# Kernel optimization log

Hardware: AMD Instinct MI355X
Metric: run time of the kernel (lower is better)

## Reference

```python
import jax, jax.numpy as jnp
import numpy as np

N_HEADS = 16
D_K = 64  # d_model / n_heads = 1024 / 16


def setup_inputs() -> dict:
    key = jax.random.key(0)
    ks = jax.random.split(key, 7)
    B, S, D = 4, 2048, 1024
    scale = 1.0 / np.sqrt(D)
    return {
        "Q": jax.random.normal(ks[0], (B, S, D), dtype=jnp.float32),
        "K": jax.random.normal(ks[1], (B, S, D), dtype=jnp.float32),
        "V": jax.random.normal(ks[2], (B, S, D), dtype=jnp.float32),
        # Linear weights stored as [in, out] so y = x @ W (bias=False in original).
        "WQ": jax.random.normal(ks[3], (D, D), dtype=jnp.float32) * scale,
        "WK": jax.random.normal(ks[4], (D, D), dtype=jnp.float32) * scale,
        "WV": jax.random.normal(ks[5], (D, D), dtype=jnp.float32) * scale,
        "Wfc": jax.random.normal(ks[6], (D, D), dtype=jnp.float32) * scale,
    }


def reference(Q, K, V, WQ, WK, WV, Wfc):
    B = Q.shape[0]
    # NOTE: the original uses a raw reshape [B, S, H*dk] -> [B, H, S, dk]
    # (NOT the usual view+transpose); row-major reshape reproduces it exactly.
    q = (Q @ WQ).reshape(B, N_HEADS, -1, D_K)  # [B, H, S, dk]
    k = (K @ WK).reshape(B, N_HEADS, -1, D_K)
    v = (V @ WV).reshape(B, N_HEADS, -1, D_K)
    scores = jnp.einsum("bhqd,bhkd->bhqk", q, k) / jnp.sqrt(jnp.asarray(D_K, q.dtype))
    attn = jax.nn.softmax(scores, axis=-1)
    ctx = jnp.einsum("bhqk,bhkd->bhqd", attn, v)  # [B, H, S, dk]
    ctx = jnp.transpose(ctx, (0, 2, 1, 3)).reshape(B, -1, N_HEADS * D_K)  # [B, S, D]
    return ctx @ Wfc
```

## Files before the change

kernel.cpp:

```cpp
#include <hip/hip_runtime.h>
#include <stdint.h>
#include <math.h>


typedef __attribute__((ext_vector_type(8))) short short8;
typedef __attribute__((ext_vector_type(4))) float f32x4;
typedef __attribute__((ext_vector_type(16))) float f32x16;
typedef __attribute__((ext_vector_type(2))) unsigned int u32x2;
typedef __attribute__((ext_vector_type(4))) unsigned int u32x4;
typedef __attribute__((ext_vector_type(8))) _Float16 half8;

__device__ __forceinline__ unsigned short bf16rne(float f) {
  unsigned int u = __builtin_bit_cast(unsigned int, f);
  unsigned int r = u + 0x7FFFu + ((u >> 16) & 1u);
  return (unsigned short)(r >> 16);
}

__device__ __forceinline__ void gld_lds16(const void* g, void* l) {
  typedef __attribute__((address_space(3))) unsigned int lds_u32;
  typedef const __attribute__((address_space(1))) unsigned int glb_u32;
  __builtin_amdgcn_global_load_lds((glb_u32*)(uintptr_t)g,
                                   (lds_u32*)(unsigned int)(uintptr_t)l,
                                   16, 0, 0);
}

__device__ __forceinline__ unsigned pkrtz(float a, float b) {
  auto h = __builtin_amdgcn_cvt_pkrtz(a, b);
  return __builtin_bit_cast(unsigned, h);
}

__device__ __forceinline__ float fexp2(float x) {
#if __has_builtin(__builtin_amdgcn_exp2f)
  return __builtin_amdgcn_exp2f(x);
#else
  float r;
  asm("v_exp_f32 %0, %1" : "=v"(r) : "v"(x));
  return r;
#endif
}

__global__ void convert_x_kernel(const float* __restrict__ Q,
                                 const float* __restrict__ K,
                                 const float* __restrict__ V,
                                 unsigned short* __restrict__ Xb) {
  const int z = blockIdx.y;
  const float* src = (z == 0) ? Q : (z == 1) ? K : V;
  const size_t i0 = ((size_t)blockIdx.x * 256 + threadIdx.x) * 8;
  const f32x4 a = *(const f32x4*)(src + i0);
  const f32x4 c = *(const f32x4*)(src + i0 + 4);
  u32x4 o;
  o[0] = (unsigned)bf16rne(a[0]) | ((unsigned)bf16rne(a[1]) << 16);
  o[1] = (unsigned)bf16rne(a[2]) | ((unsigned)bf16rne(a[3]) << 16);
  o[2] = (unsigned)bf16rne(c[0]) | ((unsigned)bf16rne(c[1]) << 16);
  o[3] = (unsigned)bf16rne(c[2]) | ((unsigned)bf16rne(c[3]) << 16);
  *(u32x4*)(Xb + (size_t)z * 8388608 + i0) = o;
}

__global__ void convert_w_kernel(const float* __restrict__ W0,
                                 const float* __restrict__ W1,
                                 const float* __restrict__ W2,
                                 const float* __restrict__ W3,
                                 unsigned short* __restrict__ Wt) {
  const int z = blockIdx.z;
  const float* W = (z == 0) ? W0 : (z == 1) ? W1 : (z == 2) ? W2 : W3;
  unsigned short* dst = Wt + (size_t)z * 1048576;
  __shared__ float tile[32][33];
  const int tx = threadIdx.x & 31, ty = threadIdx.x >> 5;
  const int k0 = blockIdx.x * 32, n0 = blockIdx.y * 32;
#pragma unroll
  for (int yy = 0; yy < 32; yy += 8)
    tile[ty + yy][tx] = W[(size_t)(k0 + ty + yy) * 1024 + n0 + tx];
  __syncthreads();
#pragma unroll
  for (int yy = 0; yy < 32; yy += 8)
    dst[(size_t)(n0 + ty + yy) * 1024 + k0 + tx] = bf16rne(tile[tx][ty + yy]);
}

__global__ __launch_bounds__(256, 2) void gemm_bt_kernel(
    const unsigned short* __restrict__ A, const unsigned short* __restrict__ Bt,
    unsigned short* __restrict__ Cbf, float* __restrict__ Cf32, float scaleZ0) {
  constexpr int K = 1024, N = 1024;
  const int z = blockIdx.z;
  const unsigned short* Ab = A + (size_t)z * 8192 * 1024;
  const unsigned short* Bb = Bt + (size_t)z * 1024 * 1024;
  const int tid = threadIdx.x;
  const int lane = tid & 63;
  const int w = tid >> 6;
  const int l15 = lane & 15, quad = lane >> 4;
  const int rowBase = blockIdx.x * 128;
  const int colBase = blockIdx.y * 128;
  const int wrow = (w >> 1) * 64;
  const int wcol = (w & 1) * 64;
  __shared__ __align__(16) unsigned short As[128 * 32];
  __shared__ __align__(16) unsigned short Bs[128 * 32];

  const f32x4 z4 = {0.0f, 0.0f, 0.0f, 0.0f};
  f32x4 acc[4][4];
#pragma unroll
  for (int i = 0; i < 4; i++)
#pragma unroll
    for (int j = 0; j < 4; j++) acc[i][j] = z4;

  const int s0 = tid, s1 = tid + 256;
  const int rA0 = s0 >> 2, cA0 = (s0 & 3) * 8;
  const int rA1 = s1 >> 2, cA1 = (s1 & 3) * 8;

  for (int k0 = 0; k0 < K; k0 += 32) {
    gld_lds16(Ab + (size_t)(rowBase + rA0) * K + k0 + cA0, (void*)(As + s0 * 8));
    gld_lds16(Ab + (size_t)(rowBase + rA1) * K + k0 + cA1, (void*)(As + s1 * 8));
    gld_lds16(Bb + (size_t)(colBase + rA0) * K + k0 + cA0, (void*)(Bs + s0 * 8));
    gld_lds16(Bb + (size_t)(colBase + rA1) * K + k0 + cA1, (void*)(Bs + s1 * 8));
    __syncthreads();
    short8 af[4], bfr[4];
#pragma unroll
    for (int i = 0; i < 4; i++)
      af[i] = *(const short8*)(As + (wrow + i * 16 + l15) * 32 + quad * 8);
#pragma unroll
    for (int j = 0; j < 4; j++)
      bfr[j] = *(const short8*)(Bs + (wcol + j * 16 + l15) * 32 + quad * 8);
#pragma unroll
    for (int i = 0; i < 4; i++)
#pragma unroll
      for (int j = 0; j < 4; j++)
        acc[i][j] =
            __builtin_amdgcn_mfma_f32_16x16x32_bf16(af[i], bfr[j], acc[i][j], 0, 0, 0);
    __syncthreads();
  }

  const float sc = (z == 0) ? scaleZ0 : 1.0f;
#pragma unroll
  for (int i = 0; i < 4; i++) {
#pragma unroll
    for (int j = 0; j < 4; j++) {
#pragma unroll
      for (int r = 0; r < 4; r++) {
        const int row = rowBase + wrow + i * 16 + quad * 4 + r;
        const int col = colBase + wcol + j * 16 + l15;
        const float v = acc[i][j][r] * sc;
        if (Cbf != nullptr) {
          Cbf[(size_t)z * 8192 * 1024 + (size_t)row * N + col] = bf16rne(v);
        } else {
          Cf32[(size_t)row * N + col] = v;
        }
      }
    }
  }
}

__global__ void vtrans_kernel(const unsigned short* __restrict__ linv,
                              unsigned short* __restrict__ Vt) {
  const int st = blockIdx.x, bh = blockIdx.y;
  const unsigned short* vp = linv + (size_t)bh * 131072;
  __shared__ unsigned short tile[64 * 136];
  const int tid = threadIdx.x;
#pragma unroll
  for (int it = 0; it < 4; it++) {
    const int idx = it * 256 + tid;
    const int s = idx >> 3, d0 = (idx & 7) * 8;
    const u32x4 vv = *(const u32x4*)(vp + (size_t)(st * 128 + s) * 64 + d0);
#pragma unroll
    for (int m = 0; m < 4; m++) {
      const unsigned lo = vv[m] & 0xffffu, hi = vv[m] >> 16;
      const float f0 = __builtin_bit_cast(float, lo << 16);
      const float f1 = __builtin_bit_cast(float, hi << 16);
      const _Float16 h0 = (_Float16)f0, h1 = (_Float16)f1;
      tile[(d0 + 2 * m) * 136 + s] = __builtin_bit_cast(unsigned short, h0);
      tile[(d0 + 2 * m + 1) * 136 + s] = __builtin_bit_cast(unsigned short, h1);
    }
  }
  __syncthreads();
#pragma unroll
  for (int it = 0; it < 4; it++) {
    const int idx = it * 256 + tid;
    const int d = idx >> 4, s0 = (idx & 15) * 8;
    const u32x4 o = *(const u32x4*)(tile + d * 136 + s0);
    *(u32x4*)(Vt + (size_t)bh * 131072 + (size_t)d * 2048 + st * 128 + s0) = o;
  }
}

__global__ __launch_bounds__(256, 2) void attn_kernel(
    const unsigned short* __restrict__ lin, const _Float16* __restrict__ Vt,
    unsigned short* __restrict__ ctxr) {
  const int bh = blockIdx.x;
  const int qt = blockIdx.y;
  const int b = bh >> 4, h = bh & 15;
  const int tid = threadIdx.x, lane = tid & 63, w = tid >> 6;
  const int l31 = lane & 31, hl = lane >> 5, x7 = l31 & 7;
  const size_t headOff = (size_t)(b * 2048 + h * 128) * 1024;
  const unsigned short* qp = lin + headOff;
  const unsigned short* kp = lin + 8388608 + headOff;
  const _Float16* vtp = Vt + (size_t)bh * 131072;

  __shared__ __align__(16) unsigned short smem[24576];
  unsigned short(*Ks)[4096] = (unsigned short(*)[4096])smem;
  _Float16(*Vs)[4096] = (_Float16(*)[4096])(smem + 8192);
  _Float16* Pl = (_Float16*)(smem + 16384) + w * 2048;

  const int stageV = (w >= 2);
  const int wbase = (stageV ? (w - 2) : w) * 256 + lane;
  auto stage = [&](int bufn, int key0) {
#pragma unroll
    for (int i = 0; i < 4; i++) {
      const int slot = wbase + i * 64;
      const int row = slot >> 3;
      const int seg = (slot & 7) ^ (row & 7);
      if (!stageV) {
        gld_lds16(kp + (size_t)(key0 + row) * 64 + seg * 8,
                  (void*)(&Ks[bufn][slot * 8]));
      } else {
        gld_lds16(vtp + (size_t)row * 2048 + key0 + seg * 8,
                  (void*)(&Vs[bufn][slot * 8]));
      }
    }
  };

  const int qrow0 = qt * 256 + w * 64;
  short8 bq[2][4];
#pragma unroll
  for (int qg = 0; qg < 2; qg++)
#pragma unroll
    for (int ks = 0; ks < 4; ks++)
      bq[qg][ks] = *(const short8*)(qp +
                                    (size_t)(qrow0 + qg * 32 + l31) * 64 +
                                    ks * 16 + hl * 8);

  f32x16 z16;
#pragma unroll
  for (int r = 0; r < 16; r++) z16[r] = 0.0f;
  f32x16 co[2][2] = {{z16, z16}, {z16, z16}};
  float mrun[2] = {-INFINITY, -INFINITY};
  float lrun[2] = {0.0f, 0.0f};

  stage(0, 0);
  __syncthreads();

  for (int kt = 0; kt < 32; kt++) {
    const int cur = kt & 1;
    if (kt < 31) stage(cur ^ 1, (kt + 1) * 64);

    short8 kf[2][4];
#pragma unroll
    for (int g = 0; g < 2; g++)
#pragma unroll
      for (int ks = 0; ks < 4; ks++) {
        const int slot = (g * 32 + l31) * 8 + ((2 * ks + hl) ^ x7);
        kf[g][ks] = *(const short8*)(&Ks[cur][slot * 8]);
      }

    f32x16 sacc[2][2] = {{z16, z16}, {z16, z16}};
    __builtin_amdgcn_s_setprio(1);
#pragma unroll
    for (int qg = 0; qg < 2; qg++)
#pragma unroll
      for (int g = 0; g < 2; g++)
#pragma unroll
        for (int ks = 0; ks < 4; ks++)
          sacc[qg][g] = __builtin_amdgcn_mfma_f32_32x32x16_bf16(
              kf[g][ks], bq[qg][ks], sacc[qg][g], 0, 0, 0);
    __builtin_amdgcn_s_setprio(0);

    half8 vf[2][2][2];
#pragma unroll
    for (int dt = 0; dt < 2; dt++)
#pragma unroll
      for (int g = 0; g < 2; g++)
#pragma unroll
        for (int s = 0; s < 2; s++) {
          const int slot = (dt * 32 + l31) * 8 + ((4 * g + 2 * s + hl) ^ x7);
          vf[dt][g][s] = *(const half8*)(&Vs[cur][slot * 8]);
        }

#pragma unroll
    for (int qg = 0; qg < 2; qg++) {
      float pmax;
      {
        float tm[8];
#pragma unroll
        for (int r = 0; r < 8; r++)
          tm[r] = fmaxf(fmaxf(sacc[qg][0][r], sacc[qg][0][r + 8]),
                        fmaxf(sacc[qg][1][r], sacc[qg][1][r + 8]));
        const float a0 = fmaxf(fmaxf(tm[0], tm[1]), fmaxf(tm[2], tm[3]));
        const float a1 = fmaxf(fmaxf(tm[4], tm[5]), fmaxf(tm[6], tm[7]));
        pmax = fmaxf(a0, a1);
      }
      pmax = fmaxf(pmax, __shfl_xor(pmax, 32, 64));
      if (!__all(pmax - mrun[qg] <= 8.0f)) {
        const float mnew = fmaxf(mrun[qg], pmax);
        const float a = fexp2(mrun[qg] - mnew);
        mrun[qg] = mnew;
        lrun[qg] *= a;
#pragma unroll
        for (int r = 0; r < 16; r++) {
          co[qg][0][r] *= a;
          co[qg][1][r] *= a;
        }
      }
      float ls0 = 0.0f, ls1 = 0.0f, ls2 = 0.0f, ls3 = 0.0f;
#pragma unroll
      for (int g = 0; g < 2; g++) {
#pragma unroll
        for (int r = 0; r < 16; r += 4) {
          const float p0 = fexp2(sacc[qg][g][r + 0] - mrun[qg]);
          const float p1 = fexp2(sacc[qg][g][r + 1] - mrun[qg]);
          const float p2 = fexp2(sacc[qg][g][r + 2] - mrun[qg]);
          const float p3 = fexp2(sacc[qg][g][r + 3] - mrun[qg]);
          sacc[qg][g][r + 0] = p0;
          sacc[qg][g][r + 1] = p1;
          sacc[qg][g][r + 2] = p2;
          sacc[qg][g][r + 3] = p3;
          ls0 += p0;
          ls1 += p1;
          ls2 += p2;
          ls3 += p3;
        }
      }
      lrun[qg] += (ls0 + ls1) + (ls2 + ls3);

#pragma unroll
      for (int g = 0; g < 2; g++) {
#pragma unroll
        for (int rg = 0; rg < 4; rg++) {
          u32x2 pw;
          pw[0] = pkrtz(sacc[qg][g][4 * rg + 0], sacc[qg][g][4 * rg + 1]);
          pw[1] = pkrtz(sacc[qg][g][4 * rg + 2], sacc[qg][g][4 * rg + 3]);
          *(u32x2*)(Pl + l31 * 64 + (((4 * g + rg) ^ x7) * 8) + hl * 4) = pw;
        }
        half8 pf[2];
#pragma unroll
        for (int s = 0; s < 2; s++)
          pf[s] =
              *(const half8*)(Pl + l31 * 64 + (((4 * g + 2 * s + hl) ^ x7) * 8));
        __builtin_amdgcn_s_setprio(1);
#pragma unroll
        for (int dt = 0; dt < 2; dt++)
#pragma unroll
          for (int s = 0; s < 2; s++)
            co[qg][dt] = __builtin_amdgcn_mfma_f32_32x32x16_f16(
                vf[dt][g][s], pf[s], co[qg][dt], 0, 0, 0);
        __builtin_amdgcn_s_setprio(0);
      }
    }
    __syncthreads();
  }

  unsigned short* Cw = smem + w * 4608;
#pragma unroll
  for (int qg = 0; qg < 2; qg++) {
    const float l = lrun[qg] + __shfl_xor(lrun[qg], 32, 64);
    const float inv = 1.0f / l;
#pragma unroll
    for (int dt = 0; dt < 2; dt++) {
#pragma unroll
      for (int r = 0; r < 16; r++) {
        const int d = dt * 32 + (r & 3) + 8 * (r >> 2) + 4 * hl;
        Cw[(qg * 32 + l31) * 72 + d] = bf16rne(co[qg][dt][r] * inv);
      }
    }
  }
  __syncthreads();
#pragma unroll
  for (int it = 0; it < 8; it++) {
    const int q = it * 8 + (lane >> 3);
    const int seg = lane & 7;
    const u32x4 o = *(const u32x4*)(Cw + q * 72 + seg * 8);
    *(u32x4*)(ctxr + (size_t)(b * 2048 + qrow0 + q) * 1024 + h * 64 + seg * 8) = o;
  }
}

extern "C" void kernel_launch(void* const* d_in, const int* in_sizes, int n_in,
                              void* d_out, int out_size, void* d_ws, size_t ws_size,
                              hipStream_t stream) {
  const float* Q = (const float*)d_in[0];
  const float* K = (const float*)d_in[1];
  const float* V = (const float*)d_in[2];
  const float* WQ = (const float*)d_in[3];
  const float* WK = (const float*)d_in[4];
  const float* WV = (const float*)d_in[5];
  const float* Wfc = (const float*)d_in[6];
  float* out = (float*)d_out;

  unsigned short* ws = (unsigned short*)d_ws;
  unsigned short* Xb = ws;
  unsigned short* ctxr = ws;
  unsigned short* Vt = ws + 8388608;
  unsigned short* Wt = ws + 25165824;
  unsigned short* lin = ws + 29360128;

  convert_x_kernel<<<dim3(4096, 3), 256, 0, stream>>>(Q, K, V, Xb);
  convert_w_kernel<<<dim3(32, 32, 4), 256, 0, stream>>>(WQ, WK, WV, Wfc, Wt);
  const float qscale = 0.125f * 1.4426950408889634f;
  gemm_bt_kernel<<<dim3(64, 8, 3), 256, 0, stream>>>(Xb, Wt, lin, nullptr, qscale);
  vtrans_kernel<<<dim3(16, 64), 256, 0, stream>>>(lin + 16777216, Vt);
  attn_kernel<<<dim3(64, 8), 256, 0, stream>>>(lin, (const _Float16*)Vt, ctxr);
  gemm_bt_kernel<<<dim3(64, 8, 1), 256, 0, stream>>>(ctxr, Wt + 3 * 1048576, nullptr,
                                                     out, 1.0f);
}
```

Baseline: 352.2 us.

## Widen GEMM K-tile with XOR-swizzled LDS and use max3 in softmax

The projection GEMM now stages 64-wide K tiles instead of 32, halving the number of barrier pairs per output tile. It also XOR-swizzles the 16-byte LDS segments to avoid bank conflicts on fragment reads. In the attention kernel, the first score MFMA is seeded with zero directly instead of zero-initialising accumulators, and the row-max reduction uses inline v_max3_f32 to cut VALU instruction count. The larger LDS footprint could lower occupancy.

```diff
diff --git a/kernel.cpp b/kernel.cpp
--- a/kernel.cpp
+++ b/kernel.cpp
@@ -37,6 +37,12 @@
   asm("v_exp_f32 %0, %1" : "=v"(r) : "v"(x));
   return r;
 #endif
+}
+
+__device__ __forceinline__ float max3f(float a, float b, float c) {
+  float r;
+  asm("v_max3_f32 %0, %1, %2, %3" : "=v"(r) : "v"(a), "v"(b), "v"(c));
+  return r;
 }
 
 __global__ void convert_x_kernel(const float* __restrict__ Q,
@@ -91,8 +97,8 @@
   const int colBase = blockIdx.y * 128;
   const int wrow = (w >> 1) * 64;
   const int wcol = (w & 1) * 64;
-  __shared__ __align__(16) unsigned short As[128 * 32];
-  __shared__ __align__(16) unsigned short Bs[128 * 32];
+  __shared__ __align__(16) unsigned short As[128 * 64];
+  __shared__ __align__(16) unsigned short Bs[128 * 64];
 
   const f32x4 z4 = {0.0f, 0.0f, 0.0f, 0.0f};
   f32x4 acc[4][4];
@@ -101,29 +107,43 @@
 #pragma unroll
     for (int j = 0; j < 4; j++) acc[i][j] = z4;
 
-  const int s0 = tid, s1 = tid + 256;
-  const int rA0 = s0 >> 2, cA0 = (s0 & 3) * 8;
-  const int rA1 = s1 >> 2, cA1 = (s1 & 3) * 8;
-
-  for (int k0 = 0; k0 < K; k0 += 32) {
-    gld_lds16(Ab + (size_t)(rowBase + rA0) * K + k0 + cA0, (void*)(As + s0 * 8));
-    gld_lds16(Ab + (size_t)(rowBase + rA1) * K + k0 + cA1, (void*)(As + s1 * 8));
-    gld_lds16(Bb + (size_t)(colBase + rA0) * K + k0 + cA0, (void*)(Bs + s0 * 8));
-    gld_lds16(Bb + (size_t)(colBase + rA1) * K + k0 + cA1, (void*)(Bs + s1 * 8));
+  for (int k0 = 0; k0 < K; k0 += 64) {
+#pragma unroll
+    for (int it = 0; it < 4; it++) {
+      const int slot = it * 256 + tid;
+      const int row = slot >> 3;
+      const int sseg = (slot & 7) ^ (row & 7);
+      gld_lds16(Ab + (size_t)(rowBase + row) * K + k0 + sseg * 8,
+                (void*)(As + slot * 8));
+      gld_lds16(Bb + (size_t)(colBase + row) * K + k0 + sseg * 8,
+                (void*)(Bs + slot * 8));
+    }
     __syncthreads();
-    short8 af[4], bfr[4];
-#pragma unroll
-    for (int i = 0; i < 4; i++)
-      af[i] = *(const short8*)(As + (wrow + i * 16 + l15) * 32 + quad * 8);
-#pragma unroll
-    for (int j = 0; j < 4; j++)
-      bfr[j] = *(const short8*)(Bs + (wcol + j * 16 + l15) * 32 + quad * 8);
-#pragma unroll
-    for (int i = 0; i < 4; i++)
-#pragma unroll
-      for (int j = 0; j < 4; j++)
-        acc[i][j] =
-            __builtin_amdgcn_mfma_f32_16x16x32_bf16(af[i], bfr[j], acc[i][j], 0, 0, 0);
+    short8 af[4][2], bfr[4][2];
+#pragma unroll
+    for (int i = 0; i < 4; i++) {
+      const int row = wrow + i * 16 + l15;
+#pragma unroll
+      for (int kk = 0; kk < 2; kk++)
+        af[i][kk] =
+            *(const short8*)(As + (row * 8 + ((kk * 4 + quad) ^ (row & 7))) * 8);
+    }
+#pragma unroll
+    for (int j = 0; j < 4; j++) {
+      const int row = wcol + j * 16 + l15;
+#pragma unroll
+      for (int kk = 0; kk < 2; kk++)
+        bfr[j][kk] =
+            *(const short8*)(Bs + (row * 8 + ((kk * 4 + quad) ^ (row & 7))) * 8);
+    }
+#pragma unroll
+    for (int kk = 0; kk < 2; kk++)
+#pragma unroll
+      for (int i = 0; i < 4; i++)
+#pragma unroll
+        for (int j = 0; j < 4; j++)
+          acc[i][j] = __builtin_amdgcn_mfma_f32_16x16x32_bf16(
+              af[i][kk], bfr[j][kk], acc[i][j], 0, 0, 0);
     __syncthreads();
   }
 
@@ -247,16 +267,19 @@
         kf[g][ks] = *(const short8*)(&Ks[cur][slot * 8]);
       }
 
-    f32x16 sacc[2][2] = {{z16, z16}, {z16, z16}};
+    f32x16 sacc[2][2];
     __builtin_amdgcn_s_setprio(1);
 #pragma unroll
     for (int qg = 0; qg < 2; qg++)
 #pragma unroll
-      for (int g = 0; g < 2; g++)
-#pragma unroll
-        for (int ks = 0; ks < 4; ks++)
+      for (int g = 0; g < 2; g++) {
+        sacc[qg][g] = __builtin_amdgcn_mfma_f32_32x32x16_bf16(
+            kf[g][0], bq[qg][0], z16, 0, 0, 0);
+#pragma unroll
+        for (int ks = 1; ks < 4; ks++)
           sacc[qg][g] = __builtin_amdgcn_mfma_f32_32x32x16_bf16(
               kf[g][ks], bq[qg][ks], sacc[qg][g], 0, 0, 0);
+      }
     __builtin_amdgcn_s_setprio(0);
 
     half8 vf[2][2][2];
@@ -277,11 +300,13 @@
         float tm[8];
 #pragma unroll
         for (int r = 0; r < 8; r++)
-          tm[r] = fmaxf(fmaxf(sacc[qg][0][r], sacc[qg][0][r + 8]),
-                        fmaxf(sacc[qg][1][r], sacc[qg][1][r + 8]));
-        const float a0 = fmaxf(fmaxf(tm[0], tm[1]), fmaxf(tm[2], tm[3]));
-        const float a1 = fmaxf(fmaxf(tm[4], tm[5]), fmaxf(tm[6], tm[7]));
-        pmax = fmaxf(a0, a1);
+          tm[r] = fmaxf(max3f(sacc[qg][0][r], sacc[qg][0][r + 8],
+                              sacc[qg][1][r]),
+                        sacc[qg][1][r + 8]);
+        const float a0 = max3f(tm[0], tm[1], tm[2]);
+        const float a1 = max3f(tm[3], tm[4], tm[5]);
+        const float a2 = fmaxf(tm[6], tm[7]);
+        pmax = max3f(a0, a1, a2);
       }
       pmax = fmaxf(pmax, __shfl_xor(pmax, 32, 64));
       if (!__all(pmax - mrun[qg] <= 8.0f)) {
```

After: 361.5 us. 1.03x slower.
